# Performance work log

Hardware: AMD Instinct MI355X
Metric: run time of the kernel (lower is better)

## Reference

```python
import jax, jax.numpy as jnp
import numpy as np

N = 10000       # nodes
E = 640000      # edges (before self-loops)
D_IN = 128
H1 = 128
H2 = 64
EMB = 64
NEG_SLOPE = 0.2  # PyG GATConv default


def setup_inputs() -> dict:
    key = jax.random.key(0)
    ks = jax.random.split(key, 12)
    s = 0.05
    return {
        "x": jax.random.normal(ks[0], (N, D_IN), dtype=jnp.float32),
        "edge_index": jax.random.randint(ks[1], (2, E), 0, N, dtype=jnp.int64),
        "W1": jax.random.normal(ks[2], (D_IN, H1), dtype=jnp.float32) * s,
        "a_src1": jax.random.normal(ks[3], (H1,), dtype=jnp.float32) * s,
        "a_dst1": jax.random.normal(ks[4], (H1,), dtype=jnp.float32) * s,
        "b1": jnp.zeros((H1,), dtype=jnp.float32),
        "W2": jax.random.normal(ks[5], (H1, H2), dtype=jnp.float32) * s,
        "a_src2": jax.random.normal(ks[6], (H2,), dtype=jnp.float32) * s,
        "a_dst2": jax.random.normal(ks[7], (H2,), dtype=jnp.float32) * s,
        "b2": jnp.zeros((H2,), dtype=jnp.float32),
        "Wp": jax.random.normal(ks[8], (H2, EMB), dtype=jnp.float32) * s,
        "bp": jnp.zeros((EMB,), dtype=jnp.float32),
    }


def _gat_conv(x, src, dst, W, a_src, a_dst, b):
    # x: [N, Din] -> h: [N, Dout]
    h = x @ W
    # edge-wise attention logits (PyG: alpha_src from source j, alpha_dst from target i)
    logits = jax.nn.leaky_relu((h @ a_src)[src] + (h @ a_dst)[dst], NEG_SLOPE)  # [E+N]
    # softmax over incoming edges of each destination node (numerically stable)
    m = jax.ops.segment_max(logits, dst, num_segments=N)
    e = jnp.exp(logits - m[dst])
    z = jax.ops.segment_sum(e, dst, num_segments=N)
    w = e / z[dst]                                                              # [E+N]
    # weighted scatter-add of source features into destinations
    out = jax.ops.segment_sum(w[:, None] * h[src], dst, num_segments=N)         # [N, Dout]
    return out + b


def reference(x, edge_index, W1, a_src1, a_dst1, b1, W2, a_src2, a_dst2, b2, Wp, bp):
    # add self-loops (PyG GATConv default add_self_loops=True)
    loop = jnp.arange(N, dtype=edge_index.dtype)
    ei = jnp.concatenate([edge_index, jnp.stack([loop, loop])], axis=1)
    src, dst = ei[0], ei[1]
    x1 = jax.nn.relu(_gat_conv(x, src, dst, W1, a_src1, a_dst1, b1))
    x2 = jax.nn.relu(_gat_conv(x1, src, dst, W2, a_src2, a_dst2, b2))
    return x2 @ Wp + bp  # [N, EMB]
```

## Files before the change

### kernel.cpp

```cpp
#include <hip/hip_runtime.h>
#include <hip/hip_bf16.h>

#define NNODES 10000
#define NEDGES 640000
#define NTOT   (NNODES + NEDGES)
#define D_IN 128
#define H1 128
#define H2 64
#define EMB 64

#define NBUCKET 160
#define BCAP    8192
#define CHUNK   4096
#define NCHUNK  ((NTOT + CHUNK - 1) / CHUNK)
#define NTILE   ((NNODES + 31) / 32)

typedef _Float16 half2v __attribute__((ext_vector_type(2)));
typedef _Float16 half4v __attribute__((ext_vector_type(4)));

union SMemA {
    struct { int ordered[CHUNK]; int hist[NBUCKET]; int binStart[NBUCKET];
             int bincur[NBUCKET]; int gcur[NBUCKET]; int wtmp[4]; } p1;
    struct { float A[32 * 64]; float B[64 * 128]; } g;
};

__device__ __forceinline__ void bucket_chunk(SMemA& sm, int c, const int* __restrict__ ei,
                                             int* __restrict__ bucket_cursor,
                                             int* __restrict__ bucket_arr) {
    int tid = threadIdx.x;
    int base = c * CHUNK;
    int n = NTOT - base; if (n > CHUNK) n = CHUNK;

    int rec[CHUNK / 256];
#pragma unroll
    for (int k = 0; k < CHUNK / 256; ++k) {
        int i = base + k * 256 + tid;
        int r = 0;
        if (i < NTOT) {
            int s, d;
            if (i < NEDGES) { s = ei[i]; d = ei[NEDGES + i]; }
            else            { s = d = i - NEDGES; }
            r = (d << 16) | s;
        }
        rec[k] = r;
    }

    for (int b = tid; b < NBUCKET; b += 256) sm.p1.hist[b] = 0;
    __syncthreads();
#pragma unroll
    for (int k = 0; k < CHUNK / 256; ++k) {
        int i = base + k * 256 + tid;
        if (i < NTOT) atomicAdd(&sm.p1.hist[rec[k] >> 22], 1);
    }
    __syncthreads();

    {
        int v = (tid < NBUCKET) ? sm.p1.hist[tid] : 0;
        int lane = tid & 63, w = tid >> 6;
        int inc = v;
        for (int o = 1; o < 64; o <<= 1) {
            int t = __shfl_up(inc, o, 64);
            if (lane >= o) inc += t;
        }
        if (lane == 63) sm.p1.wtmp[w] = inc;
        __syncthreads();
        int pre = 0;
        for (int i = 0; i < w; ++i) pre += sm.p1.wtmp[i];
        if (tid < NBUCKET) {
            sm.p1.binStart[tid] = pre + inc - v;
            sm.p1.bincur[tid]   = pre + inc - v;
        }
    }
    __syncthreads();

#pragma unroll
    for (int k = 0; k < CHUNK / 256; ++k) {
        int i = base + k * 256 + tid;
        if (i < NTOT) {
            int pos = atomicAdd(&sm.p1.bincur[rec[k] >> 22], 1);
            sm.p1.ordered[pos] = rec[k];
        }
    }
    __syncthreads();

    for (int b = tid; b < NBUCKET; b += 256) {
        int cc = sm.p1.hist[b];
        sm.p1.gcur[b] = cc ? atomicAdd(&bucket_cursor[b], cc) : 0;
    }
    __syncthreads();

#pragma unroll
    for (int k = 0; k < CHUNK / 256; ++k) {
        int i = k * 256 + tid;
        if (i < n) {
            int r = sm.p1.ordered[i];
            int b = r >> 22;
            bucket_arr[b * BCAP + sm.p1.gcur[b] + (i - sm.p1.binStart[b])] = r;
        }
    }
}

__device__ __forceinline__ void gemm1_tile(SMemA& sm, int t,
                                           const float* __restrict__ x,
                                           const float* __restrict__ W1,
                                           const float* __restrict__ a_src1,
                                           const float* __restrict__ a_dst1,
                                           _Float16* __restrict__ h1h,
                                           float* __restrict__ as1,
                                           float* __restrict__ ad1) {
    int tid = threadIdx.x;
    int row0 = t * 32;
    int tx = tid & 31;
    int ty = tid >> 5;
    float acc[4][4];
#pragma unroll
    for (int rr = 0; rr < 4; ++rr)
#pragma unroll
        for (int cc = 0; cc < 4; ++cc) acc[rr][cc] = 0.f;

    for (int kk = 0; kk < D_IN; kk += 64) {
        float4* Al4 = (float4*)sm.g.A;
        for (int idx = tid; idx < 32 * 16; idx += 256) {
            int r = idx >> 4, c = idx & 15;
            float4 z4 = {0.f, 0.f, 0.f, 0.f};
            Al4[idx] = (row0 + r < NNODES)
                ? ((const float4*)(x + (size_t)(row0 + r) * D_IN + kk))[c] : z4;
        }
        float4* Bl4 = (float4*)sm.g.B;
        const float4* B4 = (const float4*)(W1 + (size_t)kk * H1);
        for (int idx = tid; idx < 64 * H1 / 4; idx += 256) Bl4[idx] = B4[idx];
        __syncthreads();

        for (int k = 0; k < 64; ++k) {
            float bv[4];
            const float* Bk = &sm.g.B[k * H1 + tx * 4];
#pragma unroll
            for (int cc = 0; cc < 4; ++cc) bv[cc] = Bk[cc];
#pragma unroll
            for (int rr = 0; rr < 4; ++rr) {
                float a = sm.g.A[(ty + 8 * rr) * 64 + k];
#pragma unroll
                for (int cc = 0; cc < 4; ++cc) acc[rr][cc] = fmaf(a, bv[cc], acc[rr][cc]);
            }
        }
        __syncthreads();
    }

#pragma unroll
    for (int rr = 0; rr < 4; ++rr) {
        int gr = row0 + ty + 8 * rr;
        if (gr < NNODES) {
            half4v hv;
            hv.x = (_Float16)acc[rr][0]; hv.y = (_Float16)acc[rr][1];
            hv.z = (_Float16)acc[rr][2]; hv.w = (_Float16)acc[rr][3];
            ((half4v*)(h1h + (size_t)gr * H1))[tx] = hv;
        }
    }

    float asv[4], adv[4];
#pragma unroll
    for (int cc = 0; cc < 4; ++cc) {
        asv[cc] = a_src1[tx * 4 + cc];
        adv[cc] = a_dst1[tx * 4 + cc];
    }
#pragma unroll
    for (int rr = 0; rr < 4; ++rr) {
        float s1 = 0.f, s2 = 0.f;
#pragma unroll
        for (int cc = 0; cc < 4; ++cc) {
            s1 = fmaf(acc[rr][cc], asv[cc], s1);
            s2 = fmaf(acc[rr][cc], adv[cc], s2);
        }
#pragma unroll
        for (int o = 1; o < 32; o <<= 1) {
            s1 += __shfl_xor(s1, o, 64);
            s2 += __shfl_xor(s2, o, 64);
        }
        int gr = row0 + ty + 8 * rr;
        if (tx == 0 && gr < NNODES) { as1[gr] = s1; ad1[gr] = s2; }
    }
}

__global__ __launch_bounds__(256) void csr_gemm1_kernel(const int* __restrict__ ei,
                                                        int* __restrict__ bucket_cursor,
                                                        int* __restrict__ bucket_arr,
                                                        const float* __restrict__ x,
                                                        const float* __restrict__ W1,
                                                        const float* __restrict__ a_src1,
                                                        const float* __restrict__ a_dst1,
                                                        _Float16* __restrict__ h1h,
                                                        float* __restrict__ as1,
                                                        float* __restrict__ ad1) {
    __shared__ SMemA sm;
    int bid = blockIdx.x;
    if (bid < NCHUNK)
        bucket_chunk(sm, bid, ei, bucket_cursor, bucket_arr);
    else
        gemm1_tile(sm, bid - NCHUNK, x, W1, a_src1, a_dst1, h1h, as1, ad1);
}

__global__ __launch_bounds__(256) void build_kernel(const int* __restrict__ bucket_cursor,
                                                    const int* __restrict__ bucket_arr,
                                                    int* __restrict__ rowptr,
                                                    int* __restrict__ csr_src) {
    __shared__ int sbase[NBUCKET];
    __shared__ int wtmp[4];
    __shared__ int hist[64];
    __shared__ int bincur[64];
    int tid = threadIdx.x;
    int b = blockIdx.x;

    {
        int v = (tid < NBUCKET) ? bucket_cursor[tid] : 0;
        int lane = tid & 63, w = tid >> 6;
        int inc = v;
        for (int o = 1; o < 64; o <<= 1) {
            int t = __shfl_up(inc, o, 64);
            if (lane >= o) inc += t;
        }
        if (lane == 63) wtmp[w] = inc;
        __syncthreads();
        int pre = 0;
        for (int i = 0; i < w; ++i) pre += wtmp[i];
        if (tid < NBUCKET) sbase[tid] = pre + inc - v;
    }
    __syncthreads();

    int cnt = bucket_cursor[b];
    int base = sbase[b];
    const int* arr = bucket_arr + b * BCAP;

    if (tid < 64) hist[tid] = 0;
    __syncthreads();
    for (int i = tid; i < cnt; i += 256) atomicAdd(&hist[(arr[i] >> 16) & 63], 1);
    __syncthreads();

    if (tid < 64) {
        int v = hist[tid];
        int inc = v;
        for (int o = 1; o < 64; o <<= 1) {
            int t = __shfl_up(inc, o, 64);
            if (tid >= o) inc += t;
        }
        bincur[tid] = inc - v;
        int node = b * 64 + tid;
        if (node < NNODES) rowptr[node] = base + inc - v;
    }
    if (b == 0 && tid == 0) rowptr[NNODES] = NTOT;
    __syncthreads();

    for (int i = tid; i < cnt; i += 256) {
        int r = arr[i];
        int pos = base + atomicAdd(&bincur[(r >> 16) & 63], 1);
        csr_src[pos] = r & 0xFFFF;
    }
}

__global__ __launch_bounds__(256) void agg1_gemm2_kernel(const int* __restrict__ rowptr,
                                                         const int* __restrict__ csr_src,
                                                         const _Float16* __restrict__ h1h,
                                                         const float* __restrict__ as1,
                                                         const float* __restrict__ ad1,
                                                         const float* __restrict__ b1,
                                                         const float* __restrict__ W2,
                                                         const float* __restrict__ a_src2,
                                                         const float* __restrict__ a_dst2,
                                                         _Float16* __restrict__ h2h,
                                                         float* __restrict__ as2,
                                                         float* __restrict__ ad2) {
    __shared__ float Wlds[H1 * H2];
    __shared__ float xrow[4][H1];
    int tid = threadIdx.x;
    {
        const float4* W4 = (const float4*)W2;
        float4* Wl4 = (float4*)Wlds;
        for (int idx = tid; idx < H1 * H2 / 4; idx += 256) Wl4[idx] = W4[idx];
    }
    int wv = tid >> 6, lane = tid & 63;
    int wid = blockIdx.x * 4 + wv;
    int beg = rowptr[wid], end = rowptr[wid + 1];
    float ad_d = ad1[wid];
    float z = 0.f, acc0 = 0.f, acc1 = 0.f;
    const half2v* h1p = (const half2v*)h1h;

    for (int chunk = beg; chunk < end; chunk += 64) {
        int myj = chunk + lane;
        int cnt = end - chunk; if (cnt > 64) cnt = 64;
        int s_l = 0; float e_l = 0.f;
        if (myj < end) {
            s_l = csr_src[myj];
            float l = as1[s_l] + ad_d;
            l = (l > 0.f) ? l : 0.2f * l;
            e_l = __expf(l);
        }
        z += e_l;
        int cnt8 = (cnt + 7) & ~7;
        for (int t = 0; t < cnt8; t += 8) {
#pragma unroll
            for (int u = 0; u < 8; ++u) {
                int tt = __builtin_amdgcn_readfirstlane(t + u);
                int s = __builtin_amdgcn_readlane(s_l, tt);
                float e = __int_as_float(
                    __builtin_amdgcn_readlane(__float_as_int(e_l), tt));
                half2v hp = h1p[(size_t)s * 64 + lane];
                acc0 = fmaf(e, (float)hp.x, acc0);
                acc1 = fmaf(e, (float)hp.y, acc1);
            }
        }
    }
    for (int o = 32; o; o >>= 1) z += __shfl_xor(z, o, 64);
    float rz = 1.f / z;
    float2 bb = ((const float2*)b1)[lane];
    float v0 = fmaxf(acc0 * rz + bb.x, 0.f);
    float v1 = fmaxf(acc1 * rz + bb.y, 0.f);
    ((float2*)xrow[wv])[lane] = make_float2(v0, v1);
    __syncthreads();

    float hacc = 0.f;
    const float* xr = xrow[wv];
    for (int k = 0; k < H1; k += 4) {
        float4 xq = *(const float4*)&xr[k];
        hacc = fmaf(xq.x, Wlds[(k + 0) * H2 + lane], hacc);
        hacc = fmaf(xq.y, Wlds[(k + 1) * H2 + lane], hacc);
        hacc = fmaf(xq.z, Wlds[(k + 2) * H2 + lane], hacc);
        hacc = fmaf(xq.w, Wlds[(k + 3) * H2 + lane], hacc);
    }
    float s1 = hacc * a_src2[lane];
    float s2 = hacc * a_dst2[lane];
    for (int o = 32; o; o >>= 1) {
        s1 += __shfl_xor(s1, o, 64);
        s2 += __shfl_xor(s2, o, 64);
    }
    if (lane == 0) { as2[wid] = s1; ad2[wid] = s2; }
    h2h[(size_t)wid * H2 + lane] = (_Float16)hacc;
}

__global__ __launch_bounds__(256) void agg2_proj_kernel(const int* __restrict__ rowptr,
                                                        const int* __restrict__ csr_src,
                                                        const _Float16* __restrict__ h2h,
                                                        const float* __restrict__ as2,
                                                        const float* __restrict__ ad2,
                                                        const float* __restrict__ b2,
                                                        const float* __restrict__ Wp,
                                                        const float* __restrict__ bp,
                                                        float* __restrict__ out) {
    __shared__ float Wlds[H2 * EMB];
    __shared__ float xrow[4][H2];
    int tid = threadIdx.x;
    {
        const float4* W4 = (const float4*)Wp;
        float4* Wl4 = (float4*)Wlds;
        for (int idx = tid; idx < H2 * EMB / 4; idx += 256) Wl4[idx] = W4[idx];
    }
    int wv = tid >> 6, lane = tid & 63;
    int wid = blockIdx.x * 4 + wv;
    int beg = rowptr[wid], end = rowptr[wid + 1];
    float ad_d = ad2[wid];
    float z = 0.f, acc = 0.f;

    for (int chunk = beg; chunk < end; chunk += 64) {
        int myj = chunk + lane;
        int cnt = end - chunk; if (cnt > 64) cnt = 64;
        int s_l = 0; float e_l = 0.f;
        if (myj < end) {
            s_l = csr_src[myj];
            float l = as2[s_l] + ad_d;
            l = (l > 0.f) ? l : 0.2f * l;
            e_l = __expf(l);
        }
        z += e_l;
        int cnt8 = (cnt + 7) & ~7;
        for (int t = 0; t < cnt8; t += 8) {
#pragma unroll
            for (int u = 0; u < 8; ++u) {
                int tt = __builtin_amdgcn_readfirstlane(t + u);
                int s = __builtin_amdgcn_readlane(s_l, tt);
                float e = __int_as_float(
                    __builtin_amdgcn_readlane(__float_as_int(e_l), tt));
                acc = fmaf(e, (float)h2h[(size_t)s * H2 + lane], acc);
            }
        }
    }
    for (int o = 32; o; o >>= 1) z += __shfl_xor(z, o, 64);
    float x2v = fmaxf(acc * (1.f / z) + b2[lane], 0.f);
    xrow[wv][lane] = x2v;
    __syncthreads();

    float oacc = 0.f;
    const float* xr = xrow[wv];
    for (int k = 0; k < H2; k += 4) {
        float4 xq = *(const float4*)&xr[k];
        oacc = fmaf(xq.x, Wlds[(k + 0) * EMB + lane], oacc);
        oacc = fmaf(xq.y, Wlds[(k + 1) * EMB + lane], oacc);
        oacc = fmaf(xq.z, Wlds[(k + 2) * EMB + lane], oacc);
        oacc = fmaf(xq.w, Wlds[(k + 3) * EMB + lane], oacc);
    }
    out[(size_t)wid * EMB + lane] = oacc + bp[lane];
}


extern "C" void kernel_launch(void* const* d_in, const int* in_sizes, int n_in,
                              void* d_out, int out_size, void* d_ws, size_t ws_size,
                              hipStream_t stream) {
    const float* x      = (const float*)d_in[0];
    const int*   ei     = (const int*)d_in[1];
    const float* W1     = (const float*)d_in[2];
    const float* a_src1 = (const float*)d_in[3];
    const float* a_dst1 = (const float*)d_in[4];
    const float* b1     = (const float*)d_in[5];
    const float* W2     = (const float*)d_in[6];
    const float* a_src2 = (const float*)d_in[7];
    const float* a_dst2 = (const float*)d_in[8];
    const float* b2     = (const float*)d_in[9];
    const float* Wp     = (const float*)d_in[10];
    const float* bp     = (const float*)d_in[11];
    float* out = (float*)d_out;

    char* ws = (char*)d_ws;
    size_t off = 0;
    auto alloc = [&](size_t bytes) {
        void* p = ws + off;
        off = (off + bytes + 255) & ~(size_t)255;
        return p;
    };
    int*      bucket_cursor = (int*)alloc(NBUCKET * 4);
    int*      bucket_arr    = (int*)alloc((size_t)NBUCKET * BCAP * 4);
    int*      rowptr  = (int*)alloc((NNODES + 1) * 4);
    int*      csr_src = (int*)alloc((size_t)NTOT * 4);
    _Float16* h1h     = (_Float16*)alloc((size_t)NNODES * H1 * 2);
    float*    as1     = (float*)alloc(NNODES * 4);
    float*    ad1     = (float*)alloc(NNODES * 4);
    _Float16* h2h     = (_Float16*)alloc((size_t)NNODES * H2 * 2);
    float*    as2     = (float*)alloc(NNODES * 4);
    float*    ad2     = (float*)alloc(NNODES * 4);
    (void)ws_size;

    const int TB = 256;
    int wave_b = NNODES / 4;

    hipMemsetAsync(bucket_cursor, 0, NBUCKET * 4, stream);

    csr_gemm1_kernel<<<NCHUNK + NTILE, TB, 0, stream>>>(
        ei, bucket_cursor, bucket_arr, x, W1, a_src1, a_dst1, h1h, as1, ad1);

    build_kernel<<<(NNODES + 63) / 64, TB, 0, stream>>>(bucket_cursor,
                                                        bucket_arr, rowptr, csr_src);

    agg1_gemm2_kernel<<<wave_b, TB, 0, stream>>>(rowptr, csr_src, h1h, as1, ad1,
                                                 b1, W2, a_src2, a_dst2,
                                                 h2h, as2, ad2);

    agg2_proj_kernel<<<wave_b, TB, 0, stream>>>(rowptr, csr_src, h2h, as2, ad2,
                                                b2, Wp, bp, out);
}
```

Baseline: 162.9 us.

## Use fp16 dot2 for per-node GEMMs and per-wave histograms in CSR build

Stores W2 and Wp in LDS as packed half2 and computes the per-node projections with fdot2 instead of fp32 FMAs. This halves LDS footprint, allowing higher occupancy hints and dropping the block barrier. The bucketing and CSR build kernels switch to per-wave privatized histograms and cursors to reduce LDS atomic contention, and gemm1 reads B with a vector load. Rounding activations and weights to fp16 adds accuracy risk.

```diff
diff --git a/kernel.cpp b/kernel.cpp
--- a/kernel.cpp
+++ b/kernel.cpp
@@ -18,9 +18,15 @@
 typedef _Float16 half2v __attribute__((ext_vector_type(2)));
 typedef _Float16 half4v __attribute__((ext_vector_type(4)));
 
+#if __has_builtin(__builtin_amdgcn_fdot2)
+#define FDOT2(a, b, c) __builtin_amdgcn_fdot2((a), (b), (c), false)
+#else
+#define FDOT2(a, b, c) ((c) + (float)(a).x * (float)(b).x + (float)(a).y * (float)(b).y)
+#endif
+
 union SMemA {
-    struct { int ordered[CHUNK]; int hist[NBUCKET]; int binStart[NBUCKET];
-             int bincur[NBUCKET]; int gcur[NBUCKET]; int wtmp[4]; } p1;
+    struct { int ordered[CHUNK]; int hist4[4][NBUCKET]; int binStart[NBUCKET];
+             int cur4[4][NBUCKET]; int gcur[NBUCKET]; int wtmp[4]; } p1;
     struct { float A[32 * 64]; float B[64 * 128]; } g;
 };
 
@@ -28,6 +34,7 @@
                                              int* __restrict__ bucket_cursor,
                                              int* __restrict__ bucket_arr) {
     int tid = threadIdx.x;
+    int wv = tid >> 6;
     int base = c * CHUNK;
     int n = NTOT - base; if (n > CHUNK) n = CHUNK;
 
@@ -45,19 +52,25 @@
         rec[k] = r;
     }
 
-    for (int b = tid; b < NBUCKET; b += 256) sm.p1.hist[b] = 0;
+    for (int b = tid; b < 4 * NBUCKET; b += 256) ((int*)sm.p1.hist4)[b] = 0;
     __syncthreads();
 #pragma unroll
     for (int k = 0; k < CHUNK / 256; ++k) {
         int i = base + k * 256 + tid;
-        if (i < NTOT) atomicAdd(&sm.p1.hist[rec[k] >> 22], 1);
-    }
-    __syncthreads();
-
+        if (i < NTOT) atomicAdd(&sm.p1.hist4[wv][rec[k] >> 22], 1);
+    }
+    __syncthreads();
+
+    int tot = 0;
     {
-        int v = (tid < NBUCKET) ? sm.p1.hist[tid] : 0;
+        int h0 = 0, h1 = 0, h2 = 0, h3 = 0;
+        if (tid < NBUCKET) {
+            h0 = sm.p1.hist4[0][tid]; h1 = sm.p1.hist4[1][tid];
+            h2 = sm.p1.hist4[2][tid]; h3 = sm.p1.hist4[3][tid];
+            tot = h0 + h1 + h2 + h3;
+        }
         int lane = tid & 63, w = tid >> 6;
-        int inc = v;
+        int inc = tot;
         for (int o = 1; o < 64; o <<= 1) {
             int t = __shfl_up(inc, o, 64);
             if (lane >= o) inc += t;
@@ -67,8 +80,12 @@
         int pre = 0;
         for (int i = 0; i < w; ++i) pre += sm.p1.wtmp[i];
         if (tid < NBUCKET) {
-            sm.p1.binStart[tid] = pre + inc - v;
-            sm.p1.bincur[tid]   = pre + inc - v;
+            int s = pre + inc - tot;
+            sm.p1.binStart[tid] = s;
+            sm.p1.cur4[0][tid] = s;
+            sm.p1.cur4[1][tid] = s + h0;
+            sm.p1.cur4[2][tid] = s + h0 + h1;
+            sm.p1.cur4[3][tid] = s + h0 + h1 + h2;
         }
     }
     __syncthreads();
@@ -77,16 +94,14 @@
     for (int k = 0; k < CHUNK / 256; ++k) {
         int i = base + k * 256 + tid;
         if (i < NTOT) {
-            int pos = atomicAdd(&sm.p1.bincur[rec[k] >> 22], 1);
+            int pos = atomicAdd(&sm.p1.cur4[wv][rec[k] >> 22], 1);
             sm.p1.ordered[pos] = rec[k];
         }
     }
     __syncthreads();
 
-    for (int b = tid; b < NBUCKET; b += 256) {
-        int cc = sm.p1.hist[b];
-        sm.p1.gcur[b] = cc ? atomicAdd(&bucket_cursor[b], cc) : 0;
-    }
+    if (tid < NBUCKET)
+        sm.p1.gcur[tid] = tot ? atomicAdd(&bucket_cursor[tid], tot) : 0;
     __syncthreads();
 
 #pragma unroll
@@ -132,15 +147,14 @@
         __syncthreads();
 
         for (int k = 0; k < 64; ++k) {
-            float bv[4];
-            const float* Bk = &sm.g.B[k * H1 + tx * 4];
-#pragma unroll
-            for (int cc = 0; cc < 4; ++cc) bv[cc] = Bk[cc];
+            float4 bv = *(const float4*)&sm.g.B[k * H1 + tx * 4];
 #pragma unroll
             for (int rr = 0; rr < 4; ++rr) {
                 float a = sm.g.A[(ty + 8 * rr) * 64 + k];
-#pragma unroll
-                for (int cc = 0; cc < 4; ++cc) acc[rr][cc] = fmaf(a, bv[cc], acc[rr][cc]);
+                acc[rr][0] = fmaf(a, bv.x, acc[rr][0]);
+                acc[rr][1] = fmaf(a, bv.y, acc[rr][1]);
+                acc[rr][2] = fmaf(a, bv.z, acc[rr][2]);
+                acc[rr][3] = fmaf(a, bv.w, acc[rr][3]);
             }
         }
         __syncthreads();
@@ -205,9 +219,10 @@
                                                     int* __restrict__ csr_src) {
     __shared__ int sbase[NBUCKET];
     __shared__ int wtmp[4];
-    __shared__ int hist[64];
-    __shared__ int bincur[64];
+    __shared__ int hist4[4][64];
+    __shared__ int cur4[4][64];
     int tid = threadIdx.x;
+    int wv = tid >> 6;
     int b = blockIdx.x;
 
     {
@@ -224,58 +239,66 @@
         for (int i = 0; i < w; ++i) pre += wtmp[i];
         if (tid < NBUCKET) sbase[tid] = pre + inc - v;
     }
+    ((int*)hist4)[tid] = 0;
     __syncthreads();
 
     int cnt = bucket_cursor[b];
     int base = sbase[b];
     const int* arr = bucket_arr + b * BCAP;
 
-    if (tid < 64) hist[tid] = 0;
-    __syncthreads();
-    for (int i = tid; i < cnt; i += 256) atomicAdd(&hist[(arr[i] >> 16) & 63], 1);
+    for (int i = tid; i < cnt; i += 256) atomicAdd(&hist4[wv][(arr[i] >> 16) & 63], 1);
     __syncthreads();
 
     if (tid < 64) {
-        int v = hist[tid];
-        int inc = v;
+        int h0 = hist4[0][tid], h1 = hist4[1][tid], h2 = hist4[2][tid], h3 = hist4[3][tid];
+        int tot = h0 + h1 + h2 + h3;
+        int inc = tot;
         for (int o = 1; o < 64; o <<= 1) {
             int t = __shfl_up(inc, o, 64);
             if (tid >= o) inc += t;
         }
-        bincur[tid] = inc - v;
+        int s = inc - tot;
+        cur4[0][tid] = s;
+        cur4[1][tid] = s + h0;
+        cur4[2][tid] = s + h0 + h1;
+        cur4[3][tid] = s + h0 + h1 + h2;
         int node = b * 64 + tid;
-        if (node < NNODES) rowptr[node] = base + inc - v;
+        if (node < NNODES) rowptr[node] = base + s;
     }
     if (b == 0 && tid == 0) rowptr[NNODES] = NTOT;
     __syncthreads();
 
     for (int i = tid; i < cnt; i += 256) {
         int r = arr[i];
-        int pos = base + atomicAdd(&bincur[(r >> 16) & 63], 1);
+        int pos = base + atomicAdd(&cur4[wv][(r >> 16) & 63], 1);
         csr_src[pos] = r & 0xFFFF;
     }
 }
 
-__global__ __launch_bounds__(256) void agg1_gemm2_kernel(const int* __restrict__ rowptr,
-                                                         const int* __restrict__ csr_src,
-                                                         const _Float16* __restrict__ h1h,
-                                                         const float* __restrict__ as1,
-                                                         const float* __restrict__ ad1,
-                                                         const float* __restrict__ b1,
-                                                         const float* __restrict__ W2,
-                                                         const float* __restrict__ a_src2,
-                                                         const float* __restrict__ a_dst2,
-                                                         _Float16* __restrict__ h2h,
-                                                         float* __restrict__ as2,
-                                                         float* __restrict__ ad2) {
-    __shared__ float Wlds[H1 * H2];
-    __shared__ float xrow[4][H1];
+__global__ __launch_bounds__(256, 8) void agg1_gemm2_kernel(const int* __restrict__ rowptr,
+                                                            const int* __restrict__ csr_src,
+                                                            const _Float16* __restrict__ h1h,
+                                                            const float* __restrict__ as1,
+                                                            const float* __restrict__ ad1,
+                                                            const float* __restrict__ b1,
+                                                            const float* __restrict__ W2,
+                                                            const float* __restrict__ a_src2,
+                                                            const float* __restrict__ a_dst2,
+                                                            _Float16* __restrict__ h2h,
+                                                            float* __restrict__ as2,
+                                                            float* __restrict__ ad2) {
+    __shared__ half2v W2h[64 * 64];
+    __shared__ half2v xh[4][64];
     int tid = threadIdx.x;
-    {
-        const float4* W4 = (const float4*)W2;
-        float4* Wl4 = (float4*)Wlds;
-        for (int idx = tid; idx < H1 * H2 / 4; idx += 256) Wl4[idx] = W4[idx];
-    }
+    for (int idx = tid; idx < 64 * 64; idx += 256) {
+        int k2 = idx >> 6, c = idx & 63;
+        half2v w;
+        w.x = (_Float16)W2[(size_t)(2 * k2) * H2 + c];
+        w.y = (_Float16)W2[(size_t)(2 * k2 + 1) * H2 + c];
+        W2h[idx] = w;
+    }
+    __syncthreads();
+
     int wv = tid >> 6, lane = tid & 63;
     int wid = blockIdx.x * 4 + wv;
     int beg = rowptr[wid], end = rowptr[wid + 1];
@@ -313,18 +336,14 @@
     float2 bb = ((const float2*)b1)[lane];
     float v0 = fmaxf(acc0 * rz + bb.x, 0.f);
     float v1 = fmaxf(acc1 * rz + bb.y, 0.f);
-    ((float2*)xrow[wv])[lane] = make_float2(v0, v1);
-    __syncthreads();
+    half2v xp; xp.x = (_Float16)v0; xp.y = (_Float16)v1;
+    xh[wv][lane] = xp;
 
     float hacc = 0.f;
-    const float* xr = xrow[wv];
-    for (int k = 0; k < H1; k += 4) {
-        float4 xq = *(const float4*)&xr[k];
-        hacc = fmaf(xq.x, Wlds[(k + 0) * H2 + lane], hacc);
-        hacc = fmaf(xq.y, Wlds[(k + 1) * H2 + lane], hacc);
-        hacc = fmaf(xq.z, Wlds[(k + 2) * H2 + lane], hacc);
-        hacc = fmaf(xq.w, Wlds[(k + 3) * H2 + lane], hacc);
-    }
+#pragma unroll 8
+    for (int k2 = 0; k2 < 64; ++k2)
+        hacc = FDOT2(xh[wv][k2], W2h[(k2 << 6) + lane], hacc);
+
     float s1 = hacc * a_src2[lane];
     float s2 = hacc * a_dst2[lane];
     for (int o = 32; o; o >>= 1) {
@@ -335,23 +354,27 @@
     h2h[(size_t)wid * H2 + lane] = (_Float16)hacc;
 }
 
-__global__ __launch_bounds__(256) void agg2_proj_kernel(const int* __restrict__ rowptr,
-                                                        const int* __restrict__ csr_src,
-                                                        const _Float16* __restrict__ h2h,
-                                                        const float* __restrict__ as2,
-                                                        const float* __restrict__ ad2,
-                                                        const float* __restrict__ b2,
-                                                        const float* __restrict__ Wp,
-                                                        const float* __restrict__ bp,
-                                                        float* __restrict__ out) {
-    __shared__ float Wlds[H2 * EMB];
-    __shared__ float xrow[4][H2];
+__global__ __launch_bounds__(256, 8) void agg2_proj_kernel(const int* __restrict__ rowptr,
+                                                           const int* __restrict__ csr_src,
+                                                           const _Float16* __restrict__ h2h,
+                                                           const float* __restrict__ as2,
+                                                           const float* __restrict__ ad2,
+                                                           const float* __restrict__ b2,
+                                                           const float* __restrict__ Wp,
+                                                           const float* __restrict__ bp,
+                                                           float* __restrict__ out) {
+    __shared__ half2v Wph[32 * 64];
+    __shared__ _Float16 xs[4][64];
     int tid = threadIdx.x;
-    {
-        const float4* W4 = (const float4*)Wp;
-        float4* Wl4 = (float4*)Wlds;
-        for (int idx = tid; idx < H2 * EMB / 4; idx += 256) Wl4[idx] = W4[idx];
-    }
+    for (int idx = tid; idx < 32 * 64; idx += 256) {
+        int k2 = idx >> 6, c = idx & 63;
+        half2v w;
+        w.x = (_Float16)Wp[(size_t)(2 * k2) * EMB + c];
+        w.y = (_Float16)Wp[(size_t)(2 * k2 + 1) * EMB + c];
+        Wph[idx] = w;
+    }
+    __syncthreads();
+
     int wv = tid >> 6, lane = tid & 63;
     int wid = blockIdx.x * 4 + wv;
     int beg = rowptr[wid], end = rowptr[wid + 1];
@@ -383,18 +406,13 @@
     }
     for (int o = 32; o; o >>= 1) z += __shfl_xor(z, o, 64);
     float x2v = fmaxf(acc * (1.f / z) + b2[lane], 0.f);
-    xrow[wv][lane] = x2v;
-    __syncthreads();
-
+    xs[wv][lane] = (_Float16)x2v;
+
+    const half2v* xp2 = (const half2v*)xs[wv];
     float oacc = 0.f;
-    const float* xr = xrow[wv];
-    for (int k = 0; k < H2; k += 4) {
-        float4 xq = *(const float4*)&xr[k];
-        oacc = fmaf(xq.x, Wlds[(k + 0) * EMB + lane], oacc);
-        oacc = fmaf(xq.y, Wlds[(k + 1) * EMB + lane], oacc);
-        oacc = fmaf(xq.z, Wlds[(k + 2) * EMB + lane], oacc);
-        oacc = fmaf(xq.w, Wlds[(k + 3) * EMB + lane], oacc);
-    }
+#pragma unroll 8
+    for (int k2 = 0; k2 < 32; ++k2)
+        oacc = FDOT2(xp2[k2], Wph[(k2 << 6) + lane], oacc);
     out[(size_t)wid * EMB + lane] = oacc + bp[lane];
 }
 
```

New measurement: 162.7 us. Within noise of the previous version (-0.1%).
